# Optimization experiments

Measured on AMD Instinct MI355X. Metric: run time of the kernel, lower is better.

## Reference

```python
import jax, jax.numpy as jnp
import numpy as np

B, NORM_NC, LABEL_NC, H, W, SL = 8, 256, 19, 64, 64, 512
EPS = 1e-5


def _conv5(x, w, b):
    # 5x5 'same' conv, NCHW / OIHW
    y = jax.lax.conv_general_dilated(x, w, (1, 1), [(2, 2), (2, 2)],
                                     dimension_numbers=('NCHW', 'OIHW', 'NCHW'))
    return y + b[None, :, None, None]


def _instance_norm(x):
    # InstanceNorm2d(affine=False): per-sample, per-channel over HxW, biased var
    m = x.mean(axis=(2, 3), keepdims=True)
    v = x.var(axis=(2, 3), keepdims=True)
    return (x - m) / jnp.sqrt(v + EPS)


def setup_inputs() -> dict:
    key = jax.random.key(0)
    ks = jax.random.split(key, 12)
    # one-hot semantic segmentation map (what segmap.bool() assumes in practice)
    labels = jax.random.randint(ks[0], (B, H, W), 0, LABEL_NC)
    segmap = jax.nn.one_hot(labels, LABEL_NC, axis=1, dtype=jnp.float32)  # [B,19,H,W]
    s = 0.02
    return {
        'x': jax.random.normal(ks[1], (B, NORM_NC, H, W), jnp.float32),
        'segmap': segmap,
        'style_codes': jax.random.normal(ks[2], (B, LABEL_NC, SL), jnp.float32),
        'fc_w': jax.random.normal(ks[3], (LABEL_NC, SL, SL), jnp.float32) * s,
        'fc_b': jnp.zeros((LABEL_NC, SL), jnp.float32),
        'conv_gamma_w': jax.random.normal(ks[4], (NORM_NC, SL, 5, 5), jnp.float32) * s,
        'conv_gamma_b': jnp.zeros((NORM_NC,), jnp.float32),
        'conv_beta_w': jax.random.normal(ks[5], (NORM_NC, SL, 5, 5), jnp.float32) * s,
        'conv_beta_b': jnp.zeros((NORM_NC,), jnp.float32),
        'spade_shared_w': jax.random.normal(ks[6], (512, LABEL_NC, 5, 5), jnp.float32) * s,
        'spade_shared_b': jnp.zeros((512,), jnp.float32),
        'spade_gamma_w': jax.random.normal(ks[7], (NORM_NC, 512, 5, 5), jnp.float32) * s,
        'spade_gamma_b': jnp.zeros((NORM_NC,), jnp.float32),
        'spade_beta_w': jax.random.normal(ks[8], (NORM_NC, 512, 5, 5), jnp.float32) * s,
        'spade_beta_b': jnp.zeros((NORM_NC,), jnp.float32),
        'blending_gamma': jnp.zeros((1,), jnp.float32),
        'blending_beta': jnp.zeros((1,), jnp.float32),
    }


def reference(x, segmap, style_codes, fc_w, fc_b,
              conv_gamma_w, conv_gamma_b, conv_beta_w, conv_beta_b,
              spade_shared_w, spade_shared_b,
              spade_gamma_w, spade_gamma_b, spade_beta_w, spade_beta_b,
              blending_gamma, blending_beta):
    normalized = _instance_norm(x)
    # F.interpolate(segmap, size=x.shape[2:], mode='nearest') is identity here
    # (segmap already has x's spatial size).
    mask = segmap > 0  # segmap.bool(): [B,J,H,W]
    J = mask.shape[1]

    # per-class style MLP: mu[b,j] = relu(fc_mu_j(style_codes[b,j]))
    mu = jax.nn.relu(jnp.einsum('bjd,jed->bje', style_codes, fc_w) + fc_b)  # [B,J,SL]

    # for overlapping masks; pixels with no class stay zero.
    last_idx = (J - 1) - jnp.argmax(mask[:, ::-1], axis=1)  # [B,H,W] last true j
    any_m = mask.any(axis=1)                                 # [B,H,W]
    mu_sel = mu[jnp.arange(mu.shape[0])[:, None, None], last_idx]  # [B,H,W,SL]
    middle_avg = jnp.where(any_m[..., None], mu_sel, 0.0).transpose(0, 3, 1, 2)

    gamma_avg = _conv5(middle_avg, conv_gamma_w, conv_gamma_b)
    beta_avg = _conv5(middle_avg, conv_beta_w, conv_beta_b)

    actv = jax.nn.relu(_conv5(segmap, spade_shared_w, spade_shared_b))
    gamma_spade = _conv5(actv, spade_gamma_w, spade_gamma_b)
    beta_spade = _conv5(actv, spade_beta_w, spade_beta_b)

    ga = jax.nn.sigmoid(blending_gamma)  # shape (1,) broadcasts
    ba = jax.nn.sigmoid(blending_beta)
    gamma_final = ga * gamma_avg + (1 - ga) * gamma_spade
    beta_final = ba * beta_avg + (1 - ba) * beta_spade
    return normalized * (1 + gamma_final) + beta_final
```

## Files before the change

kernel.cpp:

```cpp
#include <hip/hip_runtime.h>
#include <hip/hip_bf16.h>
#include <stdint.h>

typedef __attribute__((__ext_vector_type__(8))) __bf16 bf16x8;
typedef __attribute__((__ext_vector_type__(2))) __bf16 bf16x2;
typedef __attribute__((__ext_vector_type__(4))) float  f32x4;
typedef __attribute__((__ext_vector_type__(8))) int    v8i;

#define SCALE_A_DW 0x77777777
#define SCALE_B_DW 0x79797979

__device__ __forceinline__ void gl_lds16(const void* g, void* l) {
  __builtin_amdgcn_global_load_lds(
      (__attribute__((address_space(1))) void*)(uintptr_t)g,
      (__attribute__((address_space(3))) void*)(unsigned)(uintptr_t)l,
      16, 0, 0);
}

__global__ __launch_bounds__(256) void k_prep(
    const float* __restrict__ x, float* __restrict__ stats,
    const float* __restrict__ seg, int* __restrict__ labels,
    const float* __restrict__ cgw, const float* __restrict__ cbw,
    float* __restrict__ wpa,
    const float* __restrict__ ssw, __bf16* __restrict__ wspb,
    __bf16* __restrict__ Aav) {
  __shared__ __align__(16) char smem[16*401*4];
  int blk = blockIdx.x;
  if (blk < 2048) {
    int bc = blk;
    const float4* p = (const float4*)(x + (size_t)bc * 4096);
    float s = 0.f, ss = 0.f;
    for (int i = threadIdx.x; i < 1024; i += 256) {
      float4 v = p[i];
      s  += v.x + v.y + v.z + v.w;
      ss += v.x*v.x + v.y*v.y + v.z*v.z + v.w*v.w;
    }
    #pragma unroll
    for (int o = 32; o > 0; o >>= 1) { s += __shfl_down(s, o); ss += __shfl_down(ss, o); }
    float* sh = (float*)smem;
    int wv = threadIdx.x >> 6;
    if ((threadIdx.x & 63) == 0) { sh[wv] = s; sh[4 + wv] = ss; }
    __syncthreads();
    if (threadIdx.x == 0) {
      float S = sh[0]+sh[1]+sh[2]+sh[3], SS = sh[4]+sh[5]+sh[6]+sh[7];
      float m = S * (1.f/4096.f);
      float var = SS * (1.f/4096.f) - m*m;
      stats[bc] = m;
      stats[2048 + bc] = rsqrtf(var + 1e-5f);
    }
  } else if (blk < 2176) {
    int idx = (blk - 2048)*256 + threadIdx.x;
    int b = idx >> 12, pix = idx & 4095;
    const float* p = seg + (size_t)b*19*4096 + pix;
    int lab = -1;
    for (int j = 0; j < 19; ++j) if (p[(size_t)j*4096] > 0.f) lab = j;
    labels[idx] = lab;
  } else if (blk < 3200) {
    int bid = blk - 2176;
    float* s = (float*)smem;
    int n0 = (bid & 31) * 16, c0 = (bid >> 5) * 16;
    for (int i = threadIdx.x; i < 6400; i += 256) {
      int nn = i / 400, qq = i % 400;
      int n = n0 + nn;
      const float* src = (n < 256) ? cgw + (size_t)n*12800 : cbw + (size_t)(n-256)*12800;
      s[nn*401 + qq] = src[c0*25 + qq];
    }
    __syncthreads();
    for (int i = threadIdx.x; i < 6400; i += 256) {
      int nn = i & 15, rest = i >> 4;
      int k5 = rest % 25, cc = rest / 25;
      wpa[((size_t)k5*512 + c0 + cc)*512 + n0 + nn] = s[nn*401 + cc*25 + k5];
    }
  } else if (blk < 4200) {
    int idx = (blk - 3200)*256 + threadIdx.x;
    int o = idx & 511, k5 = (idx >> 9) % 25, j = idx / 12800;
    wspb[idx] = (j < 19) ? (__bf16)ssw[((size_t)o*19 + j)*25 + k5] : (__bf16)0.f;
  } else {
    ((unsigned*)(Aav + 3800ull*512))[threadIdx.x] = 0;
  }
}

__global__ __launch_bounds__(512) void k_mu(const float* __restrict__ sc,
                                            const float* __restrict__ fcw,
                                            const float* __restrict__ fcb,
                                            float* __restrict__ mu) {
  int b = blockIdx.x / 19, j = blockIdx.x % 19;
  __shared__ float s[512];
  s[threadIdx.x] = sc[(b*19 + j)*512 + threadIdx.x];
  __syncthreads();
  int e = threadIdx.x;
  const float4* w4 = (const float4*)(fcw + ((size_t)(j*512 + e))*512);
  const float4* s4 = (const float4*)s;
  float acc = 0.f;
  for (int d = 0; d < 128; ++d) {
    float4 w = w4[d], v = s4[d];
    acc += w.x*v.x + w.y*v.y + w.z*v.z + w.w*v.w;
  }
  acc += fcb[j*512 + e];
  mu[(b*19 + j)*512 + e] = fmaxf(acc, 0.f);
}

__global__ __launch_bounds__(256) void k_pack_spade(
    const float* __restrict__ g, const float* __restrict__ bt,
    uint8_t* __restrict__ wq) {
  int n = blockIdx.x;
  const float* src = (n < 256) ? g + (size_t)n*12800 : bt + (size_t)(n-256)*12800;
  __shared__ float s[12800];
  for (int i = threadIdx.x; i < 12800; i += 256) s[i] = src[i];
  __syncthreads();
  int t = threadIdx.x;
  for (int k5 = 0; k5 < 25; ++k5) {
    float w0 = s[(2*t)*25 + k5] * 64.f, w1 = s[(2*t+1)*25 + k5] * 64.f;
    int pk = __builtin_amdgcn_cvt_pk_fp8_f32(w0, w1, 0, false);
    *(unsigned short*)(wq + ((size_t)k5*512 + n)*512 + 2*t) = (unsigned short)pk;
  }
}

__global__ __launch_bounds__(512) void k_A_avg(const float* __restrict__ mu,
                                               const float* __restrict__ wpa,
                                               __bf16* __restrict__ A) {
  int b = blockIdx.x / 25, k5 = blockIdx.x % 25;
  int n = threadIdx.x;
  const float* wp = wpa + (size_t)k5*262144 + n;
  const float* mub = mu + b*19*512;
  float acc[19];
  #pragma unroll
  for (int j = 0; j < 19; ++j) acc[j] = 0.f;
  for (int c = 0; c < 512; ++c) {
    float w = wp[(size_t)c*512];
    #pragma unroll
    for (int j = 0; j < 19; ++j) acc[j] += mub[j*512 + c] * w;
  }
  #pragma unroll
  for (int j = 0; j < 19; ++j)
    A[((size_t)((b*19 + j)*25 + k5))*512 + n] = (__bf16)acc[j];
}

__global__ void k_actv(const int* __restrict__ labels, const __bf16* __restrict__ wsp,
                       const float* __restrict__ ssb, uint8_t* __restrict__ actv) {
  int b = blockIdx.x / 68, hp = blockIdx.x % 68;
  int t = threadIdx.x;
  size_t rowbase = ((size_t)b*68 + hp)*68;
  if (hp < 2 || hp >= 66) {
    unsigned* dp = (unsigned*)(actv + rowbase*512);
    for (int i = t; i < 8704; i += 256) dp[i] = 0;
    return;
  }
  int h = hp - 2;
  __shared__ int lab[5*68];
  for (int i = t; i < 5*68; i += 256) {
    int dh = i / 68, xx = i % 68;
    int hh = h + dh - 2, ww = xx - 2;
    int l = 19;
    if (hh >= 0 && hh < 64 && ww >= 0 && ww < 64) {
      int l0 = labels[b*4096 + hh*64 + ww];
      if (l0 >= 0) l = l0;
    }
    lab[i] = l;
  }
  {
    unsigned* dp = (unsigned*)(actv + rowbase*512);
    dp[t] = 0; dp[66*128 + t] = 0;
  }
  __syncthreads();
  float bs0 = ssb[2*t], bs1 = ssb[2*t + 1];
  for (int w = 0; w < 64; ++w) {
    float a0 = bs0, a1 = bs1;
    #pragma unroll
    for (int tap = 0; tap < 25; ++tap) {
      int l = lab[(tap/5)*68 + w + (tap%5)];
      bf16x2 v = *(const bf16x2*)(wsp + (size_t)(l*25 + tap)*512 + 2*t);
      a0 += (float)v[0]; a1 += (float)v[1];
    }
    a0 = fmaxf(a0, 0.f) * 256.f;
    a1 = fmaxf(a1, 0.f) * 256.f;
    int pk = __builtin_amdgcn_cvt_pk_fp8_f32(a0, a1, 0, false);
    *(unsigned short*)(actv + (rowbase + 2 + w)*512 + 2*t) = (unsigned short)pk;
  }
}

__global__ __launch_bounds__(256) void k_conv(
    const uint8_t* __restrict__ actv, const uint8_t* __restrict__ wq,
    const float* __restrict__ sgb, const float* __restrict__ sbb,
    __bf16* __restrict__ gbs) {
  __shared__ __align__(16) uint8_t ldsA[16384];
  __shared__ __align__(16) uint8_t ldsB[16384];
  const int tid = threadIdx.x, wv = tid >> 6, lane = tid & 63;
  const int l15 = lane & 15, q = lane >> 4;
  const int m0 = blockIdx.x * 128, n0 = blockIdx.y * 128;
  const int b = m0 >> 12;

  int aoff[4], boff[4];
  #pragma unroll
  for (int i = 0; i < 4; ++i) {
    int p = (wv*4 + i)*64 + lane;
    int r = p >> 3, pc = p & 7;
    int cl = pc ^ (r & 7);
    int pix = (m0 + r) & 4095;
    int h = pix >> 6, w = pix & 63;
    aoff[i] = ((b*68 + h)*68 + w)*512 + cl*16;
    boff[i] = (n0 + r)*512 + cl*16;
  }

  const int wm = (wv >> 1) * 64, wn = (wv & 1) * 64;
  f32x4 acc[4][4] = {};

  for (int k5 = 0; k5 < 25; ++k5) {
    const int kh = k5/5, kw = k5%5;
    const int a_k = (kh*68 + kw)*512;
    const size_t b_k = (size_t)k5*262144;

    #pragma unroll
    for (int kc = 0; kc < 4; ++kc) {
      #pragma unroll
      for (int i = 0; i < 4; ++i) {
        gl_lds16(actv + aoff[i] + a_k + kc*128, ldsA + (wv*4 + i)*1024);
        gl_lds16(wq   + boff[i] + b_k + kc*128, ldsB + (wv*4 + i)*1024);
      }
      __syncthreads();
      v8i bfr[4];
      #pragma unroll
      for (int ni = 0; ni < 4; ++ni) {
        int row = wn + ni*16 + l15;
        const uint8_t* base = ldsB + row*128;
        union { v8i v; uint4 u[2]; } tt;
        tt.u[0] = *(const uint4*)(base + ((2*q    ) ^ (row & 7))*16);
        tt.u[1] = *(const uint4*)(base + ((2*q + 1) ^ (row & 7))*16);
        bfr[ni] = tt.v;
      }
      #pragma unroll
      for (int mi = 0; mi < 4; ++mi) {
        int row = wm + mi*16 + l15;
        const uint8_t* base = ldsA + row*128;
        union { v8i v; uint4 u[2]; } tt;
        tt.u[0] = *(const uint4*)(base + ((2*q    ) ^ (row & 7))*16);
        tt.u[1] = *(const uint4*)(base + ((2*q + 1) ^ (row & 7))*16);
        v8i af = tt.v;
        #pragma unroll
        for (int ni = 0; ni < 4; ++ni)
          acc[mi][ni] = __builtin_amdgcn_mfma_scale_f32_16x16x128_f8f6f4(
              af, bfr[ni], acc[mi][ni], 0, 0, 0, SCALE_A_DW, 0, SCALE_B_DW);
      }
      __syncthreads();
    }
  }

  #pragma unroll
  for (int ni = 0; ni < 4; ++ni) {
    int n = n0 + wn + ni*16 + l15;
    float bias = (n < 256) ? sgb[n] : sbb[n - 256];
    #pragma unroll
    for (int mi = 0; mi < 4; ++mi) {
      int m = m0 + wm + mi*16 + q*4;
      size_t base = (size_t)m*512 + n;
      #pragma unroll
      for (int r = 0; r < 4; ++r)
        gbs[base + (size_t)r*512] = (__bf16)(acc[mi][ni][r] + bias);
    }
  }
}

__global__ void k_gather(const int* __restrict__ labels, const __bf16* __restrict__ A,
                         const float* __restrict__ cgb, const float* __restrict__ cbb,
                         __bf16* __restrict__ gba) {
  int wt = blockIdx.x & 3, h = (blockIdx.x >> 2) & 63, b = blockIdx.x >> 8;
  int w0 = wt * 16;
  __shared__ int rowbase[5*20];
  for (int i = threadIdx.x; i < 100; i += 256) {
    int dh = i / 20, xx = i % 20;
    int hh = h + dh - 2, ww = w0 + xx - 2;
    int l = (hh >= 0 && hh < 64 && ww >= 0 && ww < 64) ? labels[b*4096 + hh*64 + ww] : -1;
    rowbase[i] = (l >= 0) ? (b*19 + l)*25 : -1;
  }
  __syncthreads();
  int t = threadIdx.x;
  float bs0, bs1;
  if (2*t < 256) { bs0 = cgb[2*t]; bs1 = cgb[2*t + 1]; }
  else           { bs0 = cbb[2*t - 256]; bs1 = cbb[2*t - 255]; }
  for (int px = 0; px < 16; ++px) {
    float a0 = bs0, a1 = bs1;
    #pragma unroll
    for (int tap = 0; tap < 25; ++tap) {
      int rb = rowbase[(tap/5)*20 + px + (tap%5)];
      int row = (rb >= 0) ? rb + tap : 3800;
      bf16x2 v = *(const bf16x2*)(A + (size_t)row*512 + 2*t);
      a0 += (float)v[0]; a1 += (float)v[1];
    }
    size_t o = ((size_t)b*4096 + h*64 + w0 + px) * 512;
    bf16x2 r; r[0] = (__bf16)a0; r[1] = (__bf16)a1;
    *(bf16x2*)(gba + o + 2*t) = r;
  }
}

__global__ __launch_bounds__(256) void k_final(
    const float* __restrict__ x, const float* __restrict__ stats,
    const __bf16* __restrict__ gba, const __bf16* __restrict__ gbs,
    const float* __restrict__ blg, const float* __restrict__ blb,
    float* __restrict__ out) {
  __shared__ __bf16 tg_av[64*66], tb_av[64*66], tg_sp[64*66], tb_sp[64*66];
  int bidx = blockIdx.x;
  int pt = bidx & 63, ct = (bidx >> 6) & 3, b = bidx >> 8;
  int c0 = ct*64, p0 = pt*64;
  for (int i = threadIdx.x; i < 4096; i += 256) {
    int p = i >> 6, c = i & 63;
    size_t src = ((size_t)b*4096 + p0 + p)*512;
    int d = p*66 + c;
    tg_av[d] = gba[src + c0 + c];
    tb_av[d] = gba[src + 256 + c0 + c];
    tg_sp[d] = gbs[src + c0 + c];
    tb_sp[d] = gbs[src + 256 + c0 + c];
  }
  __syncthreads();
  float ga = 1.f / (1.f + expf(-blg[0]));
  float ba = 1.f / (1.f + expf(-blb[0]));
  int p = threadIdx.x & 63;
  for (int cl = threadIdx.x >> 6; cl < 64; cl += 4) {
    int c = c0 + cl;
    int bc = b*256 + c;
    float mean = stats[bc], rstd = stats[2048 + bc];
    size_t o = (size_t)bc*4096 + p0 + p;
    int d = p*66 + cl;
    float gf  = ga*(float)tg_av[d] + (1.f - ga)*(float)tg_sp[d];
    float bf_ = ba*(float)tb_av[d] + (1.f - ba)*(float)tb_sp[d];
    out[o] = (x[o] - mean)*rstd*(1.f + gf) + bf_;
  }
}

extern "C" void kernel_launch(void* const* d_in, const int* in_sizes, int n_in,
                              void* d_out, int out_size, void* d_ws, size_t ws_size,
                              hipStream_t stream) {
  const float* x    = (const float*)d_in[0];
  const float* seg  = (const float*)d_in[1];
  const float* sc   = (const float*)d_in[2];
  const float* fcw  = (const float*)d_in[3];
  const float* fcb  = (const float*)d_in[4];
  const float* cgw  = (const float*)d_in[5];
  const float* cgb  = (const float*)d_in[6];
  const float* cbw  = (const float*)d_in[7];
  const float* cbb  = (const float*)d_in[8];
  const float* ssw  = (const float*)d_in[9];
  const float* ssb  = (const float*)d_in[10];
  const float* sgw  = (const float*)d_in[11];
  const float* sgb  = (const float*)d_in[12];
  const float* sbw  = (const float*)d_in[13];
  const float* sbb  = (const float*)d_in[14];
  const float* blg  = (const float*)d_in[15];
  const float* blb  = (const float*)d_in[16];
  float* out = (float*)d_out;

  char* ws = (char*)d_ws;
  size_t off = 0;
  auto alloc = [&](size_t bytes) {
    void* p = ws + off; off += (bytes + 255) & ~(size_t)255; return p;
  };
  float*   stats = (float*)alloc(2048ull*2*4);
  int*     labels= (int*)  alloc(32768ull*4);
  float*   mu    = (float*)alloc(77824ull*4);
  __bf16*  Aav   = (__bf16*)alloc((3800ull + 1)*512*2);
  __bf16*  wspb  = (__bf16*)alloc(20ull*25*512*2);
  float*   wpa   = (float*)alloc(25ull*512*512*4);
  uint8_t* wq    = (uint8_t*)alloc(25ull*512*512);
  uint8_t* actv  = (uint8_t*)alloc(8ull*68*68*512);
  __bf16*  gba   = (__bf16*)alloc(8ull*4096*512*2);
  __bf16*  gbs   = (__bf16*)alloc(8ull*4096*512*2);

  k_prep      <<<4201, 256, 0, stream>>>(x, stats, seg, labels, cgw, cbw, wpa, ssw, wspb, Aav);
  k_mu        <<<152, 512, 0, stream>>>(sc, fcw, fcb, mu);
  k_pack_spade<<<512, 256, 0, stream>>>(sgw, sbw, wq);
  k_A_avg     <<<200, 512, 0, stream>>>(mu, wpa, Aav);
  k_actv      <<<544, 256, 0, stream>>>(labels, wspb, ssb, actv);
  k_conv      <<<dim3(256, 4), 256, 0, stream>>>(actv, wq, sgb, sbb, gbs);
  k_gather    <<<2048, 256, 0, stream>>>(labels, Aav, cgb, cbb, gba);
  k_final     <<<2048, 256, 0, stream>>>(x, stats, gba, gbs, blg, blb, out);
}
```

Baseline: 658.0 us.

## Double-buffer LDS tiles in fp8 conv GEMM to overlap loads with MFMA

The implicit-GEMM conv kernel now uses two LDS buffers for A and B. The global-to-LDS load of the next K-step is issued before the MFMA compute on the current buffer, which halves the barriers per step and hides load latency behind compute. LDS use doubles to 64KB per block, which may reduce occupancy. The global_load_lds writes are only ordered by the barrier, relying on the implicit vmcnt wait before s_barrier.

```diff
diff --git a/kernel.cpp b/kernel.cpp
--- a/kernel.cpp
+++ b/kernel.cpp
@@ -183,8 +183,8 @@
     const uint8_t* __restrict__ actv, const uint8_t* __restrict__ wq,
     const float* __restrict__ sgb, const float* __restrict__ sbb,
     __bf16* __restrict__ gbs) {
-  __shared__ __align__(16) uint8_t ldsA[16384];
-  __shared__ __align__(16) uint8_t ldsB[16384];
+  __shared__ __align__(16) uint8_t ldsA[2][16384];
+  __shared__ __align__(16) uint8_t ldsB[2][16384];
   const int tid = threadIdx.x, wv = tid >> 6, lane = tid & 63;
   const int l15 = lane & 15, q = lane >> 4;
   const int m0 = blockIdx.x * 128, n0 = blockIdx.y * 128;
@@ -205,44 +205,55 @@
   const int wm = (wv >> 1) * 64, wn = (wv & 1) * 64;
   f32x4 acc[4][4] = {};
 
-  for (int k5 = 0; k5 < 25; ++k5) {
-    const int kh = k5/5, kw = k5%5;
-    const int a_k = (kh*68 + kw)*512;
-    const size_t b_k = (size_t)k5*262144;
-
-    #pragma unroll
-    for (int kc = 0; kc < 4; ++kc) {
+  auto stage = [&](int t, int buf) {
+    int k5 = t >> 2, kc = t & 3;
+    int a_k = ((k5/5)*68 + (k5%5))*512 + kc*128;
+    int b_k = k5*262144 + kc*128;
+    uint8_t* la = &ldsA[buf][0];
+    uint8_t* lb = &ldsB[buf][0];
+    #pragma unroll
+    for (int i = 0; i < 4; ++i) {
+      gl_lds16(actv + aoff[i] + a_k, la + (wv*4 + i)*1024);
+      gl_lds16(wq   + boff[i] + b_k, lb + (wv*4 + i)*1024);
+    }
+  };
+
+  auto compute = [&](int buf) {
+    v8i bfr[4];
+    #pragma unroll
+    for (int ni = 0; ni < 4; ++ni) {
+      int row = wn + ni*16 + l15;
+      const uint8_t* base = &ldsB[buf][row*128];
+      union { v8i v; uint4 u[2]; } tt;
+      tt.u[0] = *(const uint4*)(base + ((2*q    ) ^ (row & 7))*16);
+      tt.u[1] = *(const uint4*)(base + ((2*q + 1) ^ (row & 7))*16);
+      bfr[ni] = tt.v;
+    }
+    #pragma unroll
+    for (int mi = 0; mi < 4; ++mi) {
+      int row = wm + mi*16 + l15;
+      const uint8_t* base = &ldsA[buf][row*128];
+      union { v8i v; uint4 u[2]; } tt;
+      tt.u[0] = *(const uint4*)(base + ((2*q    ) ^ (row & 7))*16);
+      tt.u[1] = *(const uint4*)(base + ((2*q + 1) ^ (row & 7))*16);
+      v8i af = tt.v;
       #pragma unroll
-      for (int i = 0; i < 4; ++i) {
-        gl_lds16(actv + aoff[i] + a_k + kc*128, ldsA + (wv*4 + i)*1024);
-        gl_lds16(wq   + boff[i] + b_k + kc*128, ldsB + (wv*4 + i)*1024);
-      }
-      __syncthreads();
-      v8i bfr[4];
-      #pragma unroll
-      for (int ni = 0; ni < 4; ++ni) {
-        int row = wn + ni*16 + l15;
-        const uint8_t* base = ldsB + row*128;
-        union { v8i v; uint4 u[2]; } tt;
-        tt.u[0] = *(const uint4*)(base + ((2*q    ) ^ (row & 7))*16);
-        tt.u[1] = *(const uint4*)(base + ((2*q + 1) ^ (row & 7))*16);
-        bfr[ni] = tt.v;
-      }
-      #pragma unroll
-      for (int mi = 0; mi < 4; ++mi) {
-        int row = wm + mi*16 + l15;
-        const uint8_t* base = ldsA + row*128;
-        union { v8i v; uint4 u[2]; } tt;
-        tt.u[0] = *(const uint4*)(base + ((2*q    ) ^ (row & 7))*16);
-        tt.u[1] = *(const uint4*)(base + ((2*q + 1) ^ (row & 7))*16);
-        v8i af = tt.v;
-        #pragma unroll
-        for (int ni = 0; ni < 4; ++ni)
-          acc[mi][ni] = __builtin_amdgcn_mfma_scale_f32_16x16x128_f8f6f4(
-              af, bfr[ni], acc[mi][ni], 0, 0, 0, SCALE_A_DW, 0, SCALE_B_DW);
-      }
-      __syncthreads();
-    }
+      for (int ni = 0; ni < 4; ++ni)
+        acc[mi][ni] = __builtin_amdgcn_mfma_scale_f32_16x16x128_f8f6f4(
+            af, bfr[ni], acc[mi][ni], 0, 0, 0, SCALE_A_DW, 0, SCALE_B_DW);
+    }
+  };
+
+  stage(0, 0);
+  __syncthreads();
+  for (int tt = 0; tt < 50; ++tt) {
+    int t = 2*tt;
+    stage(t + 1, 1);
+    compute(0);
+    __syncthreads();
+    if (tt < 49) stage(t + 2, 0);
+    compute(1);
+    __syncthreads();
   }
 
   #pragma unroll
```

Result: no change. 667.7 us (+1.5%).
